# Optimization experiments

Measured on AMD Instinct MI355X. Metric: run time of the kernel, lower is better.

## Reference

```python
import jax, jax.numpy as jnp
import numpy as np

_SAMPLING_EPS = 1e-5


def setup_inputs() -> dict:
    key = jax.random.key(0)
    k0, k1, k2, k3, k4, k5, k6 = jax.random.split(key, 7)
    T, D, V, B = 8192, 4096, 32000, 64  # total tokens, hidden, vocab, num seqs
    hidden_states = jax.random.normal(k0, (T, D), jnp.float32)
    embedding = jax.random.normal(k1, (V, D), jnp.float32) * 0.02
    last_token_indices = jnp.sort(jax.random.randint(k2, (B,), 0, T)).astype(jnp.int64)
    temperatures = jax.random.uniform(k3, (B,), jnp.float32)  # in (0,1)
    top_ps = jax.random.uniform(k4, (B,), jnp.float32)
    top_ks = jax.random.randint(k5, (B,), 1, 1000).astype(jnp.int64)
    u = jax.random.uniform(k6, (B,), jnp.float32)  # inverse-CDF sample draw
    return {
        "hidden_states": hidden_states,
        "embedding": embedding,
        "temperatures": temperatures,
        "top_ps": top_ps,
        "u": u,
        "last_token_indices": last_token_indices,
        "top_ks": top_ks,
    }


def reference(hidden_states, embedding, temperatures, top_ps, u,
              last_token_indices, top_ks):
    V = embedding.shape[0]
    # _prune_hidden_states: keep last token of each sequence -> [B, D]
    h = hidden_states[last_token_indices]
    # _get_logits: [B, V]
    logits = jnp.einsum("bd,vd->bv", h, embedding)
    # temperature scaling (temps < eps treated as 1.0, greedy handled upstream)
    temps = jnp.where(temperatures < _SAMPLING_EPS, 1.0, temperatures)
    logits = logits / temps[:, None]
    probs = jax.nn.softmax(logits.astype(jnp.float32), axis=-1)

    # sort descending once; do top-k and top-p filtering in sorted space
    order = jnp.argsort(-probs, axis=-1)                 # [B, V]
    sorted_p = jnp.take_along_axis(probs, order, axis=-1)
    k = jnp.clip(top_ks, 1, V).astype(jnp.int32)
    kth = jnp.take_along_axis(sorted_p, (k - 1)[:, None], axis=-1)  # [B,1]
    f = jnp.where(sorted_p >= kth, sorted_p, 0.0)        # top-k filter
    cum = jnp.cumsum(f, axis=-1)
    # keep index i iff cumsum up to i-1 <= top_p (first element always kept)
    keep_p = ((cum - f) <= top_ps[:, None]) | (top_ps[:, None] >= 1.0 - _SAMPLING_EPS)
    f = jnp.where(keep_p, f, 0.0)
    total = jnp.sum(f, axis=-1, keepdims=True)
    # fallback to unfiltered probs if everything got zeroed
    f = jnp.where(total > 0, f, sorted_p)
    total = jnp.sum(f, axis=-1, keepdims=True)

    # multinomial via inverse CDF in sorted space
    cdf = jnp.cumsum(f, axis=-1)
    j = jnp.sum(cdf < u[:, None] * total, axis=-1)
    j = jnp.clip(j, 0, V - 1)
    tokens = jnp.take_along_axis(order, j[:, None], axis=-1).reshape(-1)

    # filtered normalized probs back in token order (for inspection/grads)
    inv = jnp.argsort(order, axis=-1)
    probs_final = jnp.take_along_axis(f / total, inv, axis=-1)
    return tokens, probs_final
```

## Files before the change

kernel.cpp:

```cpp
#include <hip/hip_runtime.h>
#include <stdint.h>

#define D_DIM 4096
#define V_DIM 32000
#define B_SEQ 64
#define MAXC 2048
#define SPLITK 4
#define KCH 1024

typedef __attribute__((ext_vector_type(8))) short short8;
typedef __attribute__((ext_vector_type(4))) float f32x4;

#define H1_OFF     0u
#define H2_OFF     131072u
#define H3_OFF     262144u
#define LOGITS_OFF 393216u
#define PART_OFF   2441216u

#define GLD16(gsrc, ldst) \
    __builtin_amdgcn_global_load_lds((const __attribute__((address_space(1))) unsigned*)(gsrc), \
                                     (__attribute__((address_space(3))) unsigned*)(ldst), 16, 0, 0)

__device__ __forceinline__ unsigned f2key(float x) {
    unsigned u = __float_as_uint(x);
    return (u & 0x80000000u) ? ~u : (u | 0x80000000u);
}
__device__ __forceinline__ float key2f(unsigned k) {
    unsigned u = (k & 0x80000000u) ? (k & 0x7FFFFFFFu) : ~k;
    return __uint_as_float(u);
}
__device__ __forceinline__ void split3(float x, ushort& a, ushort& b, ushort& c) {
    unsigned u = __float_as_uint(x);
    a = (ushort)(u >> 16);
    float r1 = x - __uint_as_float(u & 0xFFFF0000u);
    unsigned u2 = __float_as_uint(r1);
    b = (ushort)(u2 >> 16);
    float r2 = r1 - __uint_as_float(u2 & 0xFFFF0000u);
    c = (ushort)(__float_as_uint(r2) >> 16);
}

__global__ void k_prep(const float* __restrict__ hs, const int* __restrict__ lti,
                       ushort* __restrict__ h1, ushort* __restrict__ h2,
                       ushort* __restrict__ h3) {
    int b = blockIdx.x;
    const float4* src = (const float4*)(hs + (size_t)lti[b] * D_DIM);
    ushort4* d1 = (ushort4*)(h1 + (size_t)b * D_DIM);
    ushort4* d2 = (ushort4*)(h2 + (size_t)b * D_DIM);
    ushort4* d3 = (ushort4*)(h3 + (size_t)b * D_DIM);
    for (int i = threadIdx.x; i < D_DIM / 4; i += blockDim.x) {
        float4 v = src[i];
        float x[4] = {v.x, v.y, v.z, v.w};
        ushort l1[4], l2[4], l3[4];
#pragma unroll
        for (int j = 0; j < 4; ++j) split3(x[j], l1[j], l2[j], l3[j]);
        d1[i] = make_ushort4(l1[0], l1[1], l1[2], l1[3]);
        d2[i] = make_ushort4(l2[0], l2[1], l2[2], l2[3]);
        d3[i] = make_ushort4(l3[0], l3[1], l3[2], l3[3]);
    }
}

__device__ __forceinline__ void splitB(const float4& x0, const float4& x1,
                                       short8& b1, short8& b2, short8& b3) {
    float xf[8] = {x0.x, x0.y, x0.z, x0.w, x1.x, x1.y, x1.z, x1.w};
#pragma unroll
    for (int j = 0; j < 8; ++j) {
        ushort u1, u2, u3;
        split3(xf[j], u1, u2, u3);
        b1[j] = (short)u1; b2[j] = (short)u2; b3[j] = (short)u3;
    }
}

__global__ __launch_bounds__(256, 4) void k_gemm(const ushort* __restrict__ h1,
                                                 const ushort* __restrict__ h2,
                                                 const ushort* __restrict__ h3,
                                                 const float* __restrict__ emb,
                                                 float* __restrict__ part) {
    __shared__ __align__(16) float  sB[4096];
    __shared__ __align__(16) ushort sA1[4096];
    __shared__ __align__(16) ushort sA2[4096];
    __shared__ __align__(16) ushort sA3[4096];
    const int tid = threadIdx.x;
    const int w = tid >> 6, lane = tid & 63, lrow = lane & 15, q = lane >> 4;
    const int kc = blockIdx.y;
    const int vbase = blockIdx.x * 64;
    const int vrow = vbase + w * 16 + lrow;
    const size_t kbase = (size_t)kc * KCH;

    f32x4 acc[4];
#pragma unroll
    for (int mf = 0; mf < 4; ++mf)
#pragma unroll
        for (int r = 0; r < 4; ++r) acc[mf][r] = 0.f;

    const float* srcB[4];
#pragma unroll
    for (int j = 0; j < 4; ++j) {
        int row = w * 4 + j * 16 + (lane >> 4);
        unsigned c16 = (((unsigned)(lane & 15)) << 4) ^ (((unsigned)(row & 7)) << 4);
        srcB[j] = emb + (size_t)(vbase + row) * D_DIM + kbase + (c16 >> 2);
    }
    const ushort* srcA1[2]; const ushort* srcA2[2]; const ushort* srcA3[2];
#pragma unroll
    for (int j = 0; j < 2; ++j) {
        int row = w * 8 + j * 32 + (lane >> 3);
        unsigned c16 = (((unsigned)(lane & 7)) << 4) ^ (((unsigned)(row & 7)) << 4);
        size_t off = (size_t)row * D_DIM + kbase + (c16 >> 1);
        srcA1[j] = h1 + off; srcA2[j] = h2 + off; srcA3[j] = h3 + off;
    }
    const unsigned brow = (unsigned)(w * 16 + lrow);
    const unsigned bswz = (brow & 7u) << 4;
    const char* bbase = (const char*)sB + brow * 256u;

    for (int k0 = 0; k0 < KCH; k0 += 64) {
        if (k0) __syncthreads();
#pragma unroll
        for (int j = 0; j < 4; ++j)
            GLD16(srcB[j] + k0, (char*)sB + w * 1024 + j * 4096);
#pragma unroll
        for (int j = 0; j < 2; ++j) {
            GLD16(srcA1[j] + k0, (char*)sA1 + w * 1024 + j * 4096);
            GLD16(srcA2[j] + k0, (char*)sA2 + w * 1024 + j * 4096);
            GLD16(srcA3[j] + k0, (char*)sA3 + w * 1024 + j * 4096);
        }
        __syncthreads();
#pragma unroll
        for (int s = 0; s < 2; ++s) {
            unsigned binner = (unsigned)(s * 128 + q * 32);
            float4 bf0 = *(const float4*)(bbase + (binner ^ bswz));
            float4 bf1 = *(const float4*)(bbase + ((binner + 16u) ^ bswz));
            short8 vb1, vb2, vb3;
            splitB(bf0, bf1, vb1, vb2, vb3);
#pragma unroll
            for (int mf = 0; mf < 4; ++mf) {
                unsigned arow = (unsigned)(mf * 16 + lrow);
                unsigned abyte = arow * 128u
                               + (((unsigned)(s * 64 + q * 16)) ^ ((arow & 7u) << 4));
                short8 a1 = *(const short8*)((const char*)sA1 + abyte);
                short8 a2 = *(const short8*)((const char*)sA2 + abyte);
                short8 a3 = *(const short8*)((const char*)sA3 + abyte);
                acc[mf] = __builtin_amdgcn_mfma_f32_16x16x32_bf16(a1, vb1, acc[mf], 0, 0, 0);
                acc[mf] = __builtin_amdgcn_mfma_f32_16x16x32_bf16(a1, vb2, acc[mf], 0, 0, 0);
                acc[mf] = __builtin_amdgcn_mfma_f32_16x16x32_bf16(a2, vb1, acc[mf], 0, 0, 0);
                acc[mf] = __builtin_amdgcn_mfma_f32_16x16x32_bf16(a2, vb2, acc[mf], 0, 0, 0);
                acc[mf] = __builtin_amdgcn_mfma_f32_16x16x32_bf16(a1, vb3, acc[mf], 0, 0, 0);
                acc[mf] = __builtin_amdgcn_mfma_f32_16x16x32_bf16(a3, vb1, acc[mf], 0, 0, 0);
            }
        }
    }
    float* pout = part + (size_t)kc * (B_SEQ * V_DIM);
#pragma unroll
    for (int mf = 0; mf < 4; ++mf)
#pragma unroll
        for (int r = 0; r < 4; ++r) {
            int m = mf * 16 + q * 4 + r;
            pout[(size_t)m * V_DIM + vrow] = acc[mf][r];
        }
}

__device__ __forceinline__ float4 f4add(float4 a, float4 b) {
    return make_float4(a.x + b.x, a.y + b.y, a.z + b.z, a.w + b.w);
}

__global__ void k_reduce(const float* __restrict__ part,
                         const float* __restrict__ temps,
                         float* __restrict__ logits) {
    const int b = blockIdx.y;
    float t = temps[b];
    if (t < 1e-5f) t = 1.0f;
    const float inv = 1.0f / t;
    const float4* p0 = (const float4*)(part + 0 * (size_t)(B_SEQ * V_DIM) + (size_t)b * V_DIM);
    const float4* p1 = (const float4*)(part + 1 * (size_t)(B_SEQ * V_DIM) + (size_t)b * V_DIM);
    const float4* p2 = (const float4*)(part + 2 * (size_t)(B_SEQ * V_DIM) + (size_t)b * V_DIM);
    const float4* p3 = (const float4*)(part + 3 * (size_t)(B_SEQ * V_DIM) + (size_t)b * V_DIM);
    float4* lo = (float4*)(logits + (size_t)b * V_DIM);
    for (int i = blockIdx.x * 256 + threadIdx.x; i < V_DIM / 4; i += 2048) {
        float4 s = f4add(f4add(f4add(p0[i], p1[i]), p2[i]), p3[i]);
        lo[i] = make_float4(s.x * inv, s.y * inv, s.z * inv, s.w * inv);
    }
}

__global__ void k_zero(float4* __restrict__ p) {
    size_t i = (size_t)blockIdx.x * blockDim.x + threadIdx.x;
    p[i] = make_float4(0.f, 0.f, 0.f, 0.f);
}

__global__ __launch_bounds__(512) void k_sample(const float* __restrict__ logits,
                                                const int* __restrict__ tks,
                                                const float* __restrict__ tps,
                                                const float* __restrict__ uu,
                                                float* __restrict__ out_tok,
                                                float* __restrict__ out_probs) {
    const int b = blockIdx.x, t = threadIdx.x;
    const float* lr = logits + (size_t)b * V_DIM;
    __shared__ unsigned hist[2048];
    __shared__ unsigned redu[512];
    __shared__ float redf[512];
    __shared__ unsigned long long cand[MAXC];
    __shared__ float sp[MAXC];
    __shared__ unsigned s_sel1, s_ab1, s_thr, s_nc, s_ab2, s_kthkey;
    __shared__ float s_m, s_Z, s_tot;
    __shared__ int s_cnt, s_L, s_tok, s_nk;

    int k = tks[b];
    if (k < 1) k = 1;
    if (k > V_DIM) k = V_DIM;

    for (int i = t; i < 2048; i += 512) hist[i] = 0u;
    __syncthreads();
    unsigned km = 0u;
    for (int v = t; v < V_DIM; v += 512) {
        unsigned key = f2key(lr[v]);
        km = max(km, key);
        atomicAdd(&hist[key >> 21], 1u);
    }
    redu[t] = km;
    __syncthreads();
    for (int s = 256; s > 0; s >>= 1) {
        if (t < s) redu[t] = max(redu[t], redu[t + s]);
        __syncthreads();
    }
    if (t == 0) s_m = key2f(redu[0]);
    __syncthreads();
    float m = s_m;
    redu[t] = hist[4 * t] + hist[4 * t + 1] + hist[4 * t + 2] + hist[4 * t + 3];
    __syncthreads();
    if (t == 0) {
        unsigned acc = 0; int g = 0; bool found = false;
        for (int g0 = 511; g0 >= 0 && !found; g0 -= 8) {
            unsigned v[8];
#pragma unroll
            for (int j = 0; j < 8; ++j) v[j] = redu[g0 - j];
#pragma unroll
            for (int j = 0; j < 8; ++j) {
                if (acc + v[j] >= (unsigned)k) { g = g0 - j; found = true; break; }
                acc += v[j];
            }
        }
        int sel = 4 * g;
        for (int bk = 4 * g + 3; bk >= 4 * g; --bk) {
            unsigned h = hist[bk];
            if (acc + h >= (unsigned)k) { sel = bk; break; }
            acc += h;
        }
        s_sel1 = (unsigned)sel; s_ab1 = acc;
    }
    __syncthreads();
    unsigned sel1 = s_sel1, ab1 = s_ab1;

    for (int i = t; i < 2048; i += 512) hist[i] = 0u;
    __syncthreads();
    float es = 0.f;
    for (int v = t; v < V_DIM; v += 512) {
        float f = lr[v];
        es += expf(f - m);
        unsigned key = f2key(f);
        if ((key >> 21) == sel1) atomicAdd(&hist[(key >> 10) & 2047u], 1u);
    }
    redf[t] = es;
    __syncthreads();
    for (int s = 256; s > 0; s >>= 1) {
        if (t < s) redf[t] += redf[t + s];
        __syncthreads();
    }
    if (t == 0) s_Z = redf[0];
    __syncthreads();
    redu[t] = hist[4 * t] + hist[4 * t + 1] + hist[4 * t + 2] + hist[4 * t + 3];
    __syncthreads();
    if (t == 0) {
        unsigned kk = (unsigned)k - ab1;
        unsigned acc = 0; int g = 0; bool found = false;
        for (int g0 = 511; g0 >= 0 && !found; g0 -= 8) {
            unsigned v[8];
#pragma unroll
            for (int j = 0; j < 8; ++j) v[j] = redu[g0 - j];
#pragma unroll
            for (int j = 0; j < 8; ++j) {
                if (acc + v[j] >= kk) { g = g0 - j; found = true; break; }
                acc += v[j];
            }
        }
        int sel = 4 * g;
        for (int bk = 4 * g + 3; bk >= 4 * g; --bk) {
            unsigned h = hist[bk];
            if (acc + h >= kk) { sel = bk; break; }
            acc += h;
        }
        s_ab2 = ab1 + acc;
        s_thr = (sel1 << 21) | ((unsigned)sel << 10);
        s_nc = ab1 + acc + hist[sel];
    }
    __syncthreads();
    unsigned thr = s_thr;

    if (s_nc > (unsigned)MAXC) {
        for (int i = t; i < 1024; i += 512) hist[i] = 0u;
        __syncthreads();
        for (int v = t; v < V_DIM; v += 512) {
            unsigned key = f2key(lr[v]);
            if ((key & 0xFFFFFC00u) == thr) atomicAdd(&hist[key & 1023u], 1u);
        }
        __syncthreads();
        if (t == 0) {
            unsigned kk = (unsigned)k - s_ab2;
            unsigned acc = 0; int sel = 0;
            for (int bk = 1023; bk >= 0; --bk) {
                unsigned h = hist[bk];
                if (acc + h >= kk) { sel = bk; break; }
                acc += h;
            }
            s_thr = thr | (unsigned)sel;
        }
        __syncthreads();
        thr = s_thr;
    }

    if (t == 0) s_cnt = 0;
    for (int i = t; i < MAXC; i += 512) cand[i] = 0xFFFFFFFFFFFFFFFFULL;
    __syncthreads();
    for (int v = t; v < V_DIM; v += 512) {
        unsigned key = f2key(lr[v]);
        if (key >= thr) {
            int p = atomicAdd(&s_cnt, 1);
            if (p < MAXC) cand[p] = (((unsigned long long)(~key)) << 32) | (unsigned)v;
        }
    }
    __syncthreads();
    int n = s_cnt; if (n > MAXC) n = MAXC;
    const int np2 = (n <= 1) ? 1 : (1 << (32 - __clz(n - 1)));

    for (unsigned size = 2; size <= (unsigned)np2; size <<= 1)
        for (unsigned stride = size >> 1; stride > 0; stride >>= 1) {
            for (unsigned i = t; i < (unsigned)np2; i += 512) {
                unsigned j = i ^ stride;
                if (j > i) {
                    unsigned long long a = cand[i], c = cand[j];
                    bool up = ((i & size) == 0);
                    if (up ? (a > c) : (a < c)) { cand[i] = c; cand[j] = a; }
                }
            }
            __syncthreads();
        }
    float Z = s_Z;
    for (int i = t; i < n; i += 512) {
        unsigned key = ~(unsigned)(cand[i] >> 32);
        sp[i] = expf(key2f(key) - m) / Z;
    }
    for (int i = n + t; i < MAXC; i += 512) sp[i] = 0.f;
    if (t == 0) s_kthkey = ~(unsigned)(cand[k - 1] >> 32);
    __syncthreads();

    unsigned kthkey = s_kthkey;
    int cnt = 0;
    for (int i = t; i < n; i += 512)
        if ((~(unsigned)(cand[i] >> 32)) >= kthkey) cnt++;
    redu[t] = (unsigned)cnt;
    __syncthreads();
    for (int s = 256; s > 0; s >>= 1) {
        if (t < s) redu[t] += redu[t + s];
        __syncthreads();
    }
    if (t == 0) s_nk = (int)redu[0];
    __syncthreads();

    if (t == 0) {
        float top_p = tps[b];
        bool keepall = (top_p >= 1.0f - 1e-5f);
        int limit = min(n, s_nk);
        float c = 0.f; int L = limit; bool done = false;
        for (int i0 = 0; i0 < limit && !done; i0 += 8) {
            float v[8];
#pragma unroll
            for (int j = 0; j < 8; ++j) v[j] = sp[i0 + j];
#pragma unroll
            for (int j = 0; j < 8; ++j) {
                int i = i0 + j;
                if (i >= limit) { done = true; break; }
                float cum = c + v[j];
                if (!keepall && !((cum - v[j]) <= top_p)) { L = i; done = true; break; }
                c = cum;
            }
        }
        float total = c;
        float target = uu[b] * total;
        float c2 = 0.f; int jj = L - 1; done = false;
        for (int i0 = 0; i0 < L && !done; i0 += 8) {
            float v[8];
#pragma unroll
            for (int j = 0; j < 8; ++j) v[j] = sp[i0 + j];
#pragma unroll
            for (int j = 0; j < 8; ++j) {
                int i = i0 + j;
                if (i >= L) { done = true; break; }
                c2 += v[j];
                if (!(c2 < target)) { jj = i; done = true; break; }
            }
        }
        s_tok = (int)(cand[jj] & 0xFFFFFFFFULL);
        s_L = L; s_tot = total;
        out_tok[b] = (float)s_tok;
    }
    __syncthreads();
    int L = s_L; float total = s_tot;
    for (int i = t; i < L; i += 512) {
        unsigned v = (unsigned)(cand[i] & 0xFFFFFFFFULL);
        out_probs[(size_t)b * V_DIM + v] = sp[i] / total;
    }
}

extern "C" void kernel_launch(void* const* d_in, const int* in_sizes, int n_in,
                              void* d_out, int out_size, void* d_ws, size_t ws_size,
                              hipStream_t stream) {
    const float* hs    = (const float*)d_in[0];
    const float* emb   = (const float*)d_in[1];
    const float* temps = (const float*)d_in[2];
    const float* tps   = (const float*)d_in[3];
    const float* uu    = (const float*)d_in[4];
    const int*   lti   = (const int*)d_in[5];
    const int*   tks   = (const int*)d_in[6];

    float* ws = (float*)d_ws;
    ushort* h1 = (ushort*)(ws + H1_OFF);
    ushort* h2 = (ushort*)(ws + H2_OFF);
    ushort* h3 = (ushort*)(ws + H3_OFF);
    float* logits = ws + LOGITS_OFF;
    float* part   = ws + PART_OFF;

    float* out_tok   = (float*)d_out;
    float* out_probs = (float*)d_out + B_SEQ;

    k_prep<<<B_SEQ, 256, 0, stream>>>(hs, lti, h1, h2, h3);
    k_gemm<<<dim3(V_DIM / 64, SPLITK), 256, 0, stream>>>(h1, h2, h3, emb, part);
    k_zero<<<(B_SEQ * V_DIM / 4) / 256, 256, 0, stream>>>((float4*)out_probs);
    k_reduce<<<dim3(8, B_SEQ), 256, 0, stream>>>(part, temps, logits);
    k_sample<<<B_SEQ, 512, 0, stream>>>(logits, tks, tps, uu, out_tok, out_probs);
}
```

Baseline: 311.8 us.

## Double-buffer GEMM LDS tiles and fold output zeroing into reduce

```diff
diff --git a/kernel.cpp b/kernel.cpp
--- a/kernel.cpp
+++ b/kernel.cpp
@@ -70,15 +70,15 @@
     }
 }
 
-__global__ __launch_bounds__(256, 4) void k_gemm(const ushort* __restrict__ h1,
+__global__ __launch_bounds__(256, 2) void k_gemm(const ushort* __restrict__ h1,
                                                  const ushort* __restrict__ h2,
                                                  const ushort* __restrict__ h3,
                                                  const float* __restrict__ emb,
                                                  float* __restrict__ part) {
-    __shared__ __align__(16) float  sB[4096];
-    __shared__ __align__(16) ushort sA1[4096];
-    __shared__ __align__(16) ushort sA2[4096];
-    __shared__ __align__(16) ushort sA3[4096];
+    __shared__ __align__(16) float  sB[2][4096];
+    __shared__ __align__(16) ushort sA1[2][4096];
+    __shared__ __align__(16) ushort sA2[2][4096];
+    __shared__ __align__(16) ushort sA3[2][4096];
     const int tid = threadIdx.x;
     const int w = tid >> 6, lane = tid & 63, lrow = lane & 15, q = lane >> 4;
     const int kc = blockIdx.y;
@@ -109,25 +109,36 @@
     }
     const unsigned brow = (unsigned)(w * 16 + lrow);
     const unsigned bswz = (brow & 7u) << 4;
-    const char* bbase = (const char*)sB + brow * 256u;
+    const unsigned ldst = (unsigned)(w * 1024);
+
+#define STAGE(nb, kk) do { \
+        GLD16(srcB[0] + (kk), (char*)&sB[nb][0]  + ldst + 0);     \
+        GLD16(srcB[1] + (kk), (char*)&sB[nb][0]  + ldst + 4096);  \
+        GLD16(srcB[2] + (kk), (char*)&sB[nb][0]  + ldst + 8192);  \
+        GLD16(srcB[3] + (kk), (char*)&sB[nb][0]  + ldst + 12288); \
+        GLD16(srcA1[0] + (kk), (char*)&sA1[nb][0] + ldst + 0);    \
+        GLD16(srcA1[1] + (kk), (char*)&sA1[nb][0] + ldst + 4096); \
+        GLD16(srcA2[0] + (kk), (char*)&sA2[nb][0] + ldst + 0);    \
+        GLD16(srcA2[1] + (kk), (char*)&sA2[nb][0] + ldst + 4096); \
+        GLD16(srcA3[0] + (kk), (char*)&sA3[nb][0] + ldst + 0);    \
+        GLD16(srcA3[1] + (kk), (char*)&sA3[nb][0] + ldst + 4096); \
+    } while (0)
+
+    STAGE(0, 0);
+    __syncthreads();
 
     for (int k0 = 0; k0 < KCH; k0 += 64) {
-        if (k0) __syncthreads();
-#pragma unroll
-        for (int j = 0; j < 4; ++j)
-            GLD16(srcB[j] + k0, (char*)sB + w * 1024 + j * 4096);
-#pragma unroll
-        for (int j = 0; j < 2; ++j) {
-            GLD16(srcA1[j] + k0, (char*)sA1 + w * 1024 + j * 4096);
-            GLD16(srcA2[j] + k0, (char*)sA2 + w * 1024 + j * 4096);
-            GLD16(srcA3[j] + k0, (char*)sA3 + w * 1024 + j * 4096);
-        }
-        __syncthreads();
+        const int cur = (k0 >> 6) & 1;
+        if (k0 + 64 < KCH) STAGE(cur ^ 1, k0 + 64);
+        const char* bb = (const char*)&sB[cur][0] + brow * 256u;
+        const char* a1b = (const char*)&sA1[cur][0];
+        const char* a2b = (const char*)&sA2[cur][0];
+        const char* a3b = (const char*)&sA3[cur][0];
 #pragma unroll
         for (int s = 0; s < 2; ++s) {
             unsigned binner = (unsigned)(s * 128 + q * 32);
-            float4 bf0 = *(const float4*)(bbase + (binner ^ bswz));
-            float4 bf1 = *(const float4*)(bbase + ((binner + 16u) ^ bswz));
+            float4 bf0 = *(const float4*)(bb + (binner ^ bswz));
+            float4 bf1 = *(const float4*)(bb + ((binner + 16u) ^ bswz));
             short8 vb1, vb2, vb3;
             splitB(bf0, bf1, vb1, vb2, vb3);
 #pragma unroll
@@ -135,9 +146,9 @@
                 unsigned arow = (unsigned)(mf * 16 + lrow);
                 unsigned abyte = arow * 128u
                                + (((unsigned)(s * 64 + q * 16)) ^ ((arow & 7u) << 4));
-                short8 a1 = *(const short8*)((const char*)sA1 + abyte);
-                short8 a2 = *(const short8*)((const char*)sA2 + abyte);
-                short8 a3 = *(const short8*)((const char*)sA3 + abyte);
+                short8 a1 = *(const short8*)(a1b + abyte);
+                short8 a2 = *(const short8*)(a2b + abyte);
+                short8 a3 = *(const short8*)(a3b + abyte);
                 acc[mf] = __builtin_amdgcn_mfma_f32_16x16x32_bf16(a1, vb1, acc[mf], 0, 0, 0);
                 acc[mf] = __builtin_amdgcn_mfma_f32_16x16x32_bf16(a1, vb2, acc[mf], 0, 0, 0);
                 acc[mf] = __builtin_amdgcn_mfma_f32_16x16x32_bf16(a2, vb1, acc[mf], 0, 0, 0);
@@ -146,7 +157,9 @@
                 acc[mf] = __builtin_amdgcn_mfma_f32_16x16x32_bf16(a3, vb1, acc[mf], 0, 0, 0);
             }
         }
-    }
+        __syncthreads();
+    }
+#undef STAGE
     float* pout = part + (size_t)kc * (B_SEQ * V_DIM);
 #pragma unroll
     for (int mf = 0; mf < 4; ++mf)
@@ -163,7 +176,8 @@
 
 __global__ void k_reduce(const float* __restrict__ part,
                          const float* __restrict__ temps,
-                         float* __restrict__ logits) {
+                         float* __restrict__ logits,
+                         float* __restrict__ out_probs) {
     const int b = blockIdx.y;
     float t = temps[b];
     if (t < 1e-5f) t = 1.0f;
@@ -173,15 +187,13 @@
     const float4* p2 = (const float4*)(part + 2 * (size_t)(B_SEQ * V_DIM) + (size_t)b * V_DIM);
     const float4* p3 = (const float4*)(part + 3 * (size_t)(B_SEQ * V_DIM) + (size_t)b * V_DIM);
     float4* lo = (float4*)(logits + (size_t)b * V_DIM);
+    float4* po = (float4*)(out_probs + (size_t)b * V_DIM);
+    const float4 z4 = make_float4(0.f, 0.f, 0.f, 0.f);
     for (int i = blockIdx.x * 256 + threadIdx.x; i < V_DIM / 4; i += 2048) {
         float4 s = f4add(f4add(f4add(p0[i], p1[i]), p2[i]), p3[i]);
         lo[i] = make_float4(s.x * inv, s.y * inv, s.z * inv, s.w * inv);
-    }
-}
-
-__global__ void k_zero(float4* __restrict__ p) {
-    size_t i = (size_t)blockIdx.x * blockDim.x + threadIdx.x;
-    p[i] = make_float4(0.f, 0.f, 0.f, 0.f);
+        po[i] = z4;
+    }
 }
 
 __global__ __launch_bounds__(512) void k_sample(const float* __restrict__ logits,
@@ -430,7 +442,6 @@
 
     k_prep<<<B_SEQ, 256, 0, stream>>>(hs, lti, h1, h2, h3);
     k_gemm<<<dim3(V_DIM / 64, SPLITK), 256, 0, stream>>>(h1, h2, h3, emb, part);
-    k_zero<<<(B_SEQ * V_DIM / 4) / 256, 256, 0, stream>>>((float4*)out_probs);
-    k_reduce<<<dim3(8, B_SEQ), 256, 0, stream>>>(part, temps, logits);
+    k_reduce<<<dim3(8, B_SEQ), 256, 0, stream>>>(part, temps, logits, out_probs);
     k_sample<<<B_SEQ, 512, 0, stream>>>(logits, tks, tps, uu, out_tok, out_probs);
 }
```

After: 312.7 us. No clear change (+0.3%).

## Widen GEMM tile to 128 vocab rows, fold zeroing into reduce, split prep

Applied to the files above, without the earlier changes.

```diff
diff --git a/kernel.cpp b/kernel.cpp
--- a/kernel.cpp
+++ b/kernel.cpp
@@ -42,21 +42,22 @@
 __global__ void k_prep(const float* __restrict__ hs, const int* __restrict__ lti,
                        ushort* __restrict__ h1, ushort* __restrict__ h2,
                        ushort* __restrict__ h3) {
-    int b = blockIdx.x;
+    int b = blockIdx.x >> 2;
+    int quarter = blockIdx.x & 3;
+    int base = quarter * (D_DIM / 16);
     const float4* src = (const float4*)(hs + (size_t)lti[b] * D_DIM);
     ushort4* d1 = (ushort4*)(h1 + (size_t)b * D_DIM);
     ushort4* d2 = (ushort4*)(h2 + (size_t)b * D_DIM);
     ushort4* d3 = (ushort4*)(h3 + (size_t)b * D_DIM);
-    for (int i = threadIdx.x; i < D_DIM / 4; i += blockDim.x) {
-        float4 v = src[i];
-        float x[4] = {v.x, v.y, v.z, v.w};
-        ushort l1[4], l2[4], l3[4];
-#pragma unroll
-        for (int j = 0; j < 4; ++j) split3(x[j], l1[j], l2[j], l3[j]);
-        d1[i] = make_ushort4(l1[0], l1[1], l1[2], l1[3]);
-        d2[i] = make_ushort4(l2[0], l2[1], l2[2], l2[3]);
-        d3[i] = make_ushort4(l3[0], l3[1], l3[2], l3[3]);
-    }
+    int i = base + threadIdx.x;
+    float4 v = src[i];
+    float x[4] = {v.x, v.y, v.z, v.w};
+    ushort l1[4], l2[4], l3[4];
+#pragma unroll
+    for (int j = 0; j < 4; ++j) split3(x[j], l1[j], l2[j], l3[j]);
+    d1[i] = make_ushort4(l1[0], l1[1], l1[2], l1[3]);
+    d2[i] = make_ushort4(l2[0], l2[1], l2[2], l2[3]);
+    d3[i] = make_ushort4(l3[0], l3[1], l3[2], l3[3]);
 }
 
 __device__ __forceinline__ void splitB(const float4& x0, const float4& x1,
@@ -70,31 +71,32 @@
     }
 }
 
-__global__ __launch_bounds__(256, 4) void k_gemm(const ushort* __restrict__ h1,
+__global__ __launch_bounds__(256, 2) void k_gemm(const ushort* __restrict__ h1,
                                                  const ushort* __restrict__ h2,
                                                  const ushort* __restrict__ h3,
                                                  const float* __restrict__ emb,
                                                  float* __restrict__ part) {
-    __shared__ __align__(16) float  sB[4096];
+    __shared__ __align__(16) float  sB[8192];
     __shared__ __align__(16) ushort sA1[4096];
     __shared__ __align__(16) ushort sA2[4096];
     __shared__ __align__(16) ushort sA3[4096];
     const int tid = threadIdx.x;
     const int w = tid >> 6, lane = tid & 63, lrow = lane & 15, q = lane >> 4;
     const int kc = blockIdx.y;
-    const int vbase = blockIdx.x * 64;
-    const int vrow = vbase + w * 16 + lrow;
+    const int vbase = blockIdx.x * 128;
     const size_t kbase = (size_t)kc * KCH;
 
-    f32x4 acc[4];
+    f32x4 acc[4][2];
 #pragma unroll
     for (int mf = 0; mf < 4; ++mf)
 #pragma unroll
-        for (int r = 0; r < 4; ++r) acc[mf][r] = 0.f;
-
-    const float* srcB[4];
-#pragma unroll
-    for (int j = 0; j < 4; ++j) {
+        for (int nf = 0; nf < 2; ++nf)
+#pragma unroll
+            for (int r = 0; r < 4; ++r) acc[mf][nf][r] = 0.f;
+
+    const float* srcB[8];
+#pragma unroll
+    for (int j = 0; j < 8; ++j) {
         int row = w * 4 + j * 16 + (lane >> 4);
         unsigned c16 = (((unsigned)(lane & 15)) << 4) ^ (((unsigned)(row & 7)) << 4);
         srcB[j] = emb + (size_t)(vbase + row) * D_DIM + kbase + (c16 >> 2);
@@ -107,29 +109,33 @@
         size_t off = (size_t)row * D_DIM + kbase + (c16 >> 1);
         srcA1[j] = h1 + off; srcA2[j] = h2 + off; srcA3[j] = h3 + off;
     }
-    const unsigned brow = (unsigned)(w * 16 + lrow);
-    const unsigned bswz = (brow & 7u) << 4;
-    const char* bbase = (const char*)sB + brow * 256u;
+    const unsigned ldst = (unsigned)(w * 1024);
 
     for (int k0 = 0; k0 < KCH; k0 += 64) {
         if (k0) __syncthreads();
 #pragma unroll
-        for (int j = 0; j < 4; ++j)
-            GLD16(srcB[j] + k0, (char*)sB + w * 1024 + j * 4096);
+        for (int j = 0; j < 8; ++j)
+            GLD16(srcB[j] + k0, (char*)sB + ldst + j * 4096);
 #pragma unroll
         for (int j = 0; j < 2; ++j) {
-            GLD16(srcA1[j] + k0, (char*)sA1 + w * 1024 + j * 4096);
-            GLD16(srcA2[j] + k0, (char*)sA2 + w * 1024 + j * 4096);
-            GLD16(srcA3[j] + k0, (char*)sA3 + w * 1024 + j * 4096);
+            GLD16(srcA1[j] + k0, (char*)sA1 + ldst + j * 4096);
+            GLD16(srcA2[j] + k0, (char*)sA2 + ldst + j * 4096);
+            GLD16(srcA3[j] + k0, (char*)sA3 + ldst + j * 4096);
         }
         __syncthreads();
 #pragma unroll
         for (int s = 0; s < 2; ++s) {
-            unsigned binner = (unsigned)(s * 128 + q * 32);
-            float4 bf0 = *(const float4*)(bbase + (binner ^ bswz));
-            float4 bf1 = *(const float4*)(bbase + ((binner + 16u) ^ bswz));
-            short8 vb1, vb2, vb3;
-            splitB(bf0, bf1, vb1, vb2, vb3);
+            short8 vb1[2], vb2[2], vb3[2];
+#pragma unroll
+            for (int nf = 0; nf < 2; ++nf) {
+                unsigned brow = (unsigned)(w * 32 + nf * 16 + lrow);
+                const char* bb = (const char*)sB + brow * 256u;
+                unsigned bswz = (brow & 7u) << 4;
+                unsigned binner = (unsigned)(s * 128 + q * 32);
+                float4 bf0 = *(const float4*)(bb + (binner ^ bswz));
+                float4 bf1 = *(const float4*)(bb + ((binner + 16u) ^ bswz));
+                splitB(bf0, bf1, vb1[nf], vb2[nf], vb3[nf]);
+            }
 #pragma unroll
             for (int mf = 0; mf < 4; ++mf) {
                 unsigned arow = (unsigned)(mf * 16 + lrow);
@@ -138,12 +144,15 @@
                 short8 a1 = *(const short8*)((const char*)sA1 + abyte);
                 short8 a2 = *(const short8*)((const char*)sA2 + abyte);
                 short8 a3 = *(const short8*)((const char*)sA3 + abyte);
-                acc[mf] = __builtin_amdgcn_mfma_f32_16x16x32_bf16(a1, vb1, acc[mf], 0, 0, 0);
-                acc[mf] = __builtin_amdgcn_mfma_f32_16x16x32_bf16(a1, vb2, acc[mf], 0, 0, 0);
-                acc[mf] = __builtin_amdgcn_mfma_f32_16x16x32_bf16(a2, vb1, acc[mf], 0, 0, 0);
-                acc[mf] = __builtin_amdgcn_mfma_f32_16x16x32_bf16(a2, vb2, acc[mf], 0, 0, 0);
-                acc[mf] = __builtin_amdgcn_mfma_f32_16x16x32_bf16(a1, vb3, acc[mf], 0, 0, 0);
-                acc[mf] = __builtin_amdgcn_mfma_f32_16x16x32_bf16(a3, vb1, acc[mf], 0, 0, 0);
+#pragma unroll
+                for (int nf = 0; nf < 2; ++nf) {
+                    acc[mf][nf] = __builtin_amdgcn_mfma_f32_16x16x32_bf16(a1, vb1[nf], acc[mf][nf], 0, 0, 0);
+                    acc[mf][nf] = __builtin_amdgcn_mfma_f32_16x16x32_bf16(a1, vb2[nf], acc[mf][nf], 0, 0, 0);
+                    acc[mf][nf] = __builtin_amdgcn_mfma_f32_16x16x32_bf16(a2, vb1[nf], acc[mf][nf], 0, 0, 0);
+                    acc[mf][nf] = __builtin_amdgcn_mfma_f32_16x16x32_bf16(a2, vb2[nf], acc[mf][nf], 0, 0, 0);
+                    acc[mf][nf] = __builtin_amdgcn_mfma_f32_16x16x32_bf16(a1, vb3[nf], acc[mf][nf], 0, 0, 0);
+                    acc[mf][nf] = __builtin_amdgcn_mfma_f32_16x16x32_bf16(a3, vb1[nf], acc[mf][nf], 0, 0, 0);
+                }
             }
         }
     }
@@ -153,7 +162,9 @@
 #pragma unroll
         for (int r = 0; r < 4; ++r) {
             int m = mf * 16 + q * 4 + r;
-            pout[(size_t)m * V_DIM + vrow] = acc[mf][r];
+#pragma unroll
+            for (int nf = 0; nf < 2; ++nf)
+                pout[(size_t)m * V_DIM + vbase + w * 32 + nf * 16 + lrow] = acc[mf][nf][r];
         }
 }
 
@@ -163,7 +174,8 @@
 
 __global__ void k_reduce(const float* __restrict__ part,
                          const float* __restrict__ temps,
-                         float* __restrict__ logits) {
+                         float* __restrict__ logits,
+                         float* __restrict__ out_probs) {
     const int b = blockIdx.y;
     float t = temps[b];
     if (t < 1e-5f) t = 1.0f;
@@ -173,15 +185,13 @@
     const float4* p2 = (const float4*)(part + 2 * (size_t)(B_SEQ * V_DIM) + (size_t)b * V_DIM);
     const float4* p3 = (const float4*)(part + 3 * (size_t)(B_SEQ * V_DIM) + (size_t)b * V_DIM);
     float4* lo = (float4*)(logits + (size_t)b * V_DIM);
+    float4* po = (float4*)(out_probs + (size_t)b * V_DIM);
+    const float4 z4 = make_float4(0.f, 0.f, 0.f, 0.f);
     for (int i = blockIdx.x * 256 + threadIdx.x; i < V_DIM / 4; i += 2048) {
         float4 s = f4add(f4add(f4add(p0[i], p1[i]), p2[i]), p3[i]);
         lo[i] = make_float4(s.x * inv, s.y * inv, s.z * inv, s.w * inv);
-    }
-}
-
-__global__ void k_zero(float4* __restrict__ p) {
-    size_t i = (size_t)blockIdx.x * blockDim.x + threadIdx.x;
-    p[i] = make_float4(0.f, 0.f, 0.f, 0.f);
+        po[i] = z4;
+    }
 }
 
 __global__ __launch_bounds__(512) void k_sample(const float* __restrict__ logits,
@@ -428,9 +438,8 @@
     float* out_tok   = (float*)d_out;
     float* out_probs = (float*)d_out + B_SEQ;
 
-    k_prep<<<B_SEQ, 256, 0, stream>>>(hs, lti, h1, h2, h3);
-    k_gemm<<<dim3(V_DIM / 64, SPLITK), 256, 0, stream>>>(h1, h2, h3, emb, part);
-    k_zero<<<(B_SEQ * V_DIM / 4) / 256, 256, 0, stream>>>((float4*)out_probs);
-    k_reduce<<<dim3(8, B_SEQ), 256, 0, stream>>>(part, temps, logits);
+    k_prep<<<B_SEQ * 4, 256, 0, stream>>>(hs, lti, h1, h2, h3);
+    k_gemm<<<dim3(V_DIM / 128, SPLITK), 256, 0, stream>>>(h1, h2, h3, emb, part);
+    k_reduce<<<dim3(8, B_SEQ), 256, 0, stream>>>(part, temps, logits, out_probs);
     k_sample<<<B_SEQ, 512, 0, stream>>>(logits, tks, tps, uu, out_tok, out_probs);
 }
```

New measurement: 299.4 us. 4.0% less time.
